# Optimization experiments

Measured on AMD Instinct MI355X. Metric: run time of the kernel, lower is better.

The kernel has to match this reference:

```python
import jax, jax.numpy as jnp
import numpy as np

N, M, H, K, CIN, COUT, P = 50000, 50000, 32, 15, 64, 128, 3
KP_EXTENT = 0.072
RADIUS = 0.06


def setup_inputs() -> dict:
    key = jax.random.key(0)
    ks = jax.random.split(key, 7)
    q_pts = jax.random.uniform(ks[0], (N, P), dtype=jnp.float32) * 0.05
    s_pts = jax.random.uniform(ks[1], (M, P), dtype=jnp.float32) * 0.05
    neighb_inds = jax.random.randint(ks[2], (N, H), 0, M, dtype=jnp.int64)
    x = jax.random.normal(ks[3], (M, CIN), dtype=jnp.float32)
    # kernel points inside sphere of radius RADIUS (stand-in for load_kernels)
    kernel_points = jax.random.normal(ks[4], (K, P), dtype=jnp.float32) * (0.5 * RADIUS)
    stddev = np.sqrt(1.0 / (K * COUT)).astype(np.float32)
    weights = jax.random.normal(ks[5], (K, CIN, COUT), dtype=jnp.float32) * stddev
    bias = jnp.zeros((COUT,), dtype=jnp.float32)
    return {"q_pts": q_pts, "s_pts": s_pts, "neighb_inds": neighb_inds,
            "x": x, "kernel_points": kernel_points, "weights": weights, "bias": bias}


def reference(q_pts, s_pts, neighb_inds, x, kernel_points, weights, bias):
    # pad support points with a far-away point and features with a zero row
    s_pad = jnp.concatenate([s_pts, jnp.full((1, s_pts.shape[1]), 1e6, s_pts.dtype)], axis=0)
    x_pad = jnp.concatenate([x, jnp.zeros((1, x.shape[1]), x.dtype)], axis=0)
    # gather neighbor coords/features: [N, H, P], [N, H, CIN]
    neighbors = s_pad[neighb_inds] - q_pts[:, None, :]
    neighb_x = x_pad[neighb_inds]
    # distances to kernel points: [N, H, K]
    diff = neighbors[:, :, None, :] - kernel_points  # [N, H, K, P]
    sq_d = jnp.sum(diff * diff, axis=-1)
    all_weights = jax.nn.relu(1.0 - jnp.sqrt(sq_d) / KP_EXTENT)  # linear influence
    # aggregate: [N, K, CIN] then apply per-kernel-point weights and sum over K
    weighted_features = jnp.einsum('nhk,nhc->nkc', all_weights, neighb_x)
    out = jnp.einsum('nkc,kco->no', weighted_features, weights) + bias  # [N, COUT]
    return out
```

## Files before the change

kernel.cpp:

```cpp
#include <hip/hip_runtime.h>


#define NPTS   50000
#define NPAD   50048
#define HNB    32
#define KPTS   15
#define CING   64
#define COUTG  128
#define KDIM   960
#define MSUP   50000
#define INV_EXT 13.888889f

#define X2BF_BLKS 1563
#define WT_BLKS   15
#define TWP       72

typedef __attribute__((ext_vector_type(8))) short bf16x8;
typedef __attribute__((ext_vector_type(8))) unsigned short u16x8;
typedef __attribute__((ext_vector_type(4))) float f32x4;

static __device__ __forceinline__ unsigned short f2bf(float f) {
    unsigned int u = __float_as_uint(f);
    u += 0x7FFFu + ((u >> 16) & 1u);
    return (unsigned short)(u >> 16);
}

__global__ __launch_bounds__(256) void kpconv_prep(const float* __restrict__ x,
                                                   unsigned short* __restrict__ xb,
                                                   const float* __restrict__ wgt,
                                                   unsigned short* __restrict__ Wt) {
    __shared__ unsigned short tw[128 * TWP];
    const int tid = threadIdx.x;
    if (blockIdx.x < X2BF_BLKS) {
        int i = (blockIdx.x * 256 + tid) * 8;
        if (i >= MSUP * CING) return;
        float4 a = *(const float4*)(x + i);
        float4 b = *(const float4*)(x + i + 4);
        u16x8 o;
        o[0] = f2bf(a.x); o[1] = f2bf(a.y); o[2] = f2bf(a.z); o[3] = f2bf(a.w);
        o[4] = f2bf(b.x); o[5] = f2bf(b.y); o[6] = f2bf(b.z); o[7] = f2bf(b.w);
        *(u16x8*)(xb + i) = o;
        return;
    }
    const int kc0 = (blockIdx.x - X2BF_BLKS) * 64;
#pragma unroll
    for (int it = 0; it < 32; ++it) {
        int idx = it * 256 + tid;
        int kcl = idx >> 7, o = idx & 127;
        tw[o * TWP + kcl] = f2bf(wgt[(size_t)(kc0 + kcl) * COUTG + o]);
    }
    __syncthreads();
#pragma unroll
    for (int it = 0; it < 4; ++it) {
        int idx = it * 256 + tid;
        int o = idx >> 3, c16 = idx & 7;
        uint4 v = *(const uint4*)&tw[o * TWP + c16 * 8];
        *(uint4*)&Wt[(size_t)o * KDIM + kc0 + c16 * 8] = v;
    }
}

__global__ __launch_bounds__(256, 5) void kpconv_agg4(
    const float* __restrict__ q_pts, const float* __restrict__ s_pts,
    const int* __restrict__ inds, const unsigned short* __restrict__ xb,
    const float* __restrict__ kpts, unsigned short* __restrict__ wf)
{
    __shared__ float4 nb[4 * HNB];

    const int tid  = threadIdx.x;
    const int wav  = tid >> 6;
    const int lane = tid & 63;
    const int l15  = lane & 15;
    const int quad = lane >> 4;
    const int n    = blockIdx.x * 4 + wav;

    if (lane < HNB) {
        int m = inds[n * HNB + lane];
        float qx = q_pts[n * 3 + 0];
        float qy = q_pts[n * 3 + 1];
        float qz = q_pts[n * 3 + 2];
        nb[wav * HNB + lane] = make_float4(s_pts[m * 3 + 0] - qx,
                                           s_pts[m * 3 + 1] - qy,
                                           s_pts[m * 3 + 2] - qz,
                                           __int_as_float(m));
    }
    __syncthreads();

    const bool kvalid = (l15 < KPTS);
    const int  kidx   = kvalid ? l15 : 0;
    const float kx = kpts[kidx * 3 + 0];
    const float ky = kpts[kidx * 3 + 1];
    const float kz = kpts[kidx * 3 + 2];

    bf16x8 af;
    const unsigned short* bj[8];
#pragma unroll
    for (int j = 0; j < 8; ++j) {
        float4 v = nb[wav * HNB + quad * 8 + j];
        bj[j] = xb + (((size_t)__float_as_int(v.w)) << 6) + l15;
        float dx = v.x - kx, dy = v.y - ky, dz = v.z - kz;
        float d  = sqrtf(dx * dx + dy * dy + dz * dz);
        float w  = kvalid ? fmaxf(0.f, 1.f - d * INV_EXT) : 0.f;
        af[j] = (short)f2bf(w);
    }

    unsigned int gv[32];
#pragma unroll
    for (int j = 0; j < 8; ++j)
#pragma unroll
        for (int nt = 0; nt < 4; ++nt)
            gv[j * 4 + nt] = bj[j][nt * 16];
    __builtin_amdgcn_sched_barrier(0);

    f32x4 acc[4];
#pragma unroll
    for (int nt = 0; nt < 4; ++nt) acc[nt] = (f32x4){0.f, 0.f, 0.f, 0.f};

#pragma unroll
    for (int nt = 0; nt < 4; ++nt) {
        union { unsigned int u[4]; bf16x8 f; } pk;
#pragma unroll
        for (int jj = 0; jj < 4; ++jj)
            pk.u[jj] = gv[(2 * jj) * 4 + nt] | (gv[(2 * jj + 1) * 4 + nt] << 16);
        acc[nt] = __builtin_amdgcn_mfma_f32_16x16x32_bf16(pk.f, af, acc[nt], 0, 0, 0);
    }

    if (kvalid) {
        unsigned short* wp = wf + (size_t)n * KDIM + l15 * CING + quad * 4;
#pragma unroll
        for (int nt = 0; nt < 4; ++nt) {
            unsigned int lo = (unsigned)f2bf(acc[nt][0]) | ((unsigned)f2bf(acc[nt][1]) << 16);
            unsigned int hi = (unsigned)f2bf(acc[nt][2]) | ((unsigned)f2bf(acc[nt][3]) << 16);
            *(uint2*)(wp + nt * 16) = make_uint2(lo, hi);
        }
    }
}

#define GBM 64
#define GBK 64
#define GLP 72

__global__ __launch_bounds__(256) void kpconv_gemm2(
    const unsigned short* __restrict__ A,
    const unsigned short* __restrict__ Bt,
    const float* __restrict__ bias,
    float* __restrict__ out)
{
    __shared__ unsigned short As[GBM * GLP];
    __shared__ unsigned short Bs[COUTG * GLP];

    const int tid  = threadIdx.x;
    const int wave = tid >> 6;
    const int lane = tid & 63;
    const int l15  = lane & 15;
    const int quad = lane >> 4;
    const long blockM = (long)blockIdx.x * GBM;

    f32x4 acc[8];
#pragma unroll
    for (int i = 0; i < 8; ++i) acc[i] = (f32x4){0.f, 0.f, 0.f, 0.f};

    const int arow = tid >> 2, acol = (tid & 3) * 16;
    const int brow = tid >> 1, bcol = (tid & 1) * 32;
    const unsigned short* aptr = A + (size_t)(blockM + arow) * KDIM + acol;
    const unsigned short* bptr = Bt + (size_t)brow * KDIM + bcol;

    uint4 ra0 = *(const uint4*)(aptr);
    uint4 ra1 = *(const uint4*)(aptr + 8);
    uint4 rb0 = *(const uint4*)(bptr);
    uint4 rb1 = *(const uint4*)(bptr + 8);
    uint4 rb2 = *(const uint4*)(bptr + 16);
    uint4 rb3 = *(const uint4*)(bptr + 24);

    for (int kk = 0; kk < KDIM; kk += GBK) {
        __syncthreads();
        *(uint4*)&As[arow * GLP + acol]      = ra0;
        *(uint4*)&As[arow * GLP + acol + 8]  = ra1;
        *(uint4*)&Bs[brow * GLP + bcol]      = rb0;
        *(uint4*)&Bs[brow * GLP + bcol + 8]  = rb1;
        *(uint4*)&Bs[brow * GLP + bcol + 16] = rb2;
        *(uint4*)&Bs[brow * GLP + bcol + 24] = rb3;
        __syncthreads();

        if (kk + GBK < KDIM) {
            ra0 = *(const uint4*)(aptr + kk + GBK);
            ra1 = *(const uint4*)(aptr + kk + GBK + 8);
            rb0 = *(const uint4*)(bptr + kk + GBK);
            rb1 = *(const uint4*)(bptr + kk + GBK + 8);
            rb2 = *(const uint4*)(bptr + kk + GBK + 16);
            rb3 = *(const uint4*)(bptr + kk + GBK + 24);
        }

#pragma unroll
        for (int ch = 0; ch < 2; ++ch) {
            bf16x8 afr = *(bf16x8*)&As[(wave * 16 + l15) * GLP + ch * 32 + quad * 8];
#pragma unroll
            for (int nf = 0; nf < 8; ++nf) {
                bf16x8 bfr = *(bf16x8*)&Bs[(nf * 16 + l15) * GLP + ch * 32 + quad * 8];
                acc[nf] = __builtin_amdgcn_mfma_f32_16x16x32_bf16(afr, bfr, acc[nf], 0, 0, 0);
            }
        }
    }

    const long r0 = blockM + wave * 16 + quad * 4;
#pragma unroll
    for (int nf = 0; nf < 8; ++nf) {
        const int col = nf * 16 + l15;
        const float bv = bias[col];
#pragma unroll
        for (int r = 0; r < 4; ++r) {
            long row = r0 + r;
            if (row < NPTS) out[row * COUTG + col] = acc[nf][r] + bv;
        }
    }
}

extern "C" void kernel_launch(void* const* d_in, const int* in_sizes, int n_in,
                              void* d_out, int out_size, void* d_ws, size_t ws_size,
                              hipStream_t stream) {
    const float* q_pts = (const float*)d_in[0];
    const float* s_pts = (const float*)d_in[1];
    const int*   inds  = (const int*)d_in[2];
    const float* x     = (const float*)d_in[3];
    const float* kpts  = (const float*)d_in[4];
    const float* wgt   = (const float*)d_in[5];
    const float* bias  = (const float*)d_in[6];
    float* out = (float*)d_out;

    unsigned short* wfp = (unsigned short*)d_ws;
    unsigned short* xb  = wfp + (size_t)NPAD * KDIM;
    unsigned short* Wt  = xb + (size_t)MSUP * CING;

    kpconv_prep<<<X2BF_BLKS + WT_BLKS, 256, 0, stream>>>(x, xb, wgt, Wt);
    kpconv_agg4<<<NPTS / 4, 256, 0, stream>>>(q_pts, s_pts, inds, xb, kpts, wfp);
    kpconv_gemm2<<<NPAD / GBM, 256, 0, stream>>>(wfp, Wt, bias, out);
}
```

Before: 168.3 us.

## Stage gathered neighbor features into LDS via direct global-to-LDS loads

```diff
diff --git a/kernel.cpp b/kernel.cpp
--- a/kernel.cpp
+++ b/kernel.cpp
@@ -23,6 +23,13 @@
     unsigned int u = __float_as_uint(f);
     u += 0x7FFFu + ((u >> 16) & 1u);
     return (unsigned short)(u >> 16);
+}
+
+static __device__ __forceinline__ void gload_lds16(const unsigned short* g,
+                                                   unsigned short* l) {
+    __builtin_amdgcn_global_load_lds(
+        (const __attribute__((address_space(1))) void*)g,
+        (__attribute__((address_space(3))) void*)l, 16, 0, 0);
 }
 
 __global__ __launch_bounds__(256) void kpconv_prep(const float* __restrict__ x,
@@ -59,12 +66,14 @@
     }
 }
 
-__global__ __launch_bounds__(256, 5) void kpconv_agg4(
+__global__ __launch_bounds__(256, 8) void kpconv_agg5(
     const float* __restrict__ q_pts, const float* __restrict__ s_pts,
     const int* __restrict__ inds, const unsigned short* __restrict__ xb,
     const float* __restrict__ kpts, unsigned short* __restrict__ wf)
 {
     __shared__ float4 nb[4 * HNB];
+    __shared__ int    midx[4 * HNB];
+    __shared__ unsigned short xs[4 * HNB * 64];
 
     const int tid  = threadIdx.x;
     const int wav  = tid >> 6;
@@ -75,15 +84,27 @@
 
     if (lane < HNB) {
         int m = inds[n * HNB + lane];
+        midx[wav * HNB + lane] = m;
         float qx = q_pts[n * 3 + 0];
         float qy = q_pts[n * 3 + 1];
         float qz = q_pts[n * 3 + 2];
         nb[wav * HNB + lane] = make_float4(s_pts[m * 3 + 0] - qx,
                                            s_pts[m * 3 + 1] - qy,
                                            s_pts[m * 3 + 2] - qz,
-                                           __int_as_float(m));
+                                           0.f);
     }
     __syncthreads();
+
+    unsigned short* xsw = &xs[wav * (HNB * 64)];
+    {
+        const int hsub = lane >> 3;
+        const int c0   = (lane & 7) * 8;
+#pragma unroll
+        for (int i = 0; i < 4; ++i) {
+            int m = midx[wav * HNB + i * 8 + hsub];
+            gload_lds16(xb + (((size_t)m) << 6) + c0, xsw + i * 8 * 64);
+        }
+    }
 
     const bool kvalid = (l15 < KPTS);
     const int  kidx   = kvalid ? l15 : 0;
@@ -92,23 +113,16 @@
     const float kz = kpts[kidx * 3 + 2];
 
     bf16x8 af;
-    const unsigned short* bj[8];
 #pragma unroll
     for (int j = 0; j < 8; ++j) {
         float4 v = nb[wav * HNB + quad * 8 + j];
-        bj[j] = xb + (((size_t)__float_as_int(v.w)) << 6) + l15;
         float dx = v.x - kx, dy = v.y - ky, dz = v.z - kz;
         float d  = sqrtf(dx * dx + dy * dy + dz * dz);
         float w  = kvalid ? fmaxf(0.f, 1.f - d * INV_EXT) : 0.f;
         af[j] = (short)f2bf(w);
     }
 
-    unsigned int gv[32];
-#pragma unroll
-    for (int j = 0; j < 8; ++j)
-#pragma unroll
-        for (int nt = 0; nt < 4; ++nt)
-            gv[j * 4 + nt] = bj[j][nt * 16];
+    asm volatile("s_waitcnt vmcnt(0)" ::: "memory");
     __builtin_amdgcn_sched_barrier(0);
 
     f32x4 acc[4];
@@ -119,8 +133,11 @@
     for (int nt = 0; nt < 4; ++nt) {
         union { unsigned int u[4]; bf16x8 f; } pk;
 #pragma unroll
-        for (int jj = 0; jj < 4; ++jj)
-            pk.u[jj] = gv[(2 * jj) * 4 + nt] | (gv[(2 * jj + 1) * 4 + nt] << 16);
+        for (int jj = 0; jj < 4; ++jj) {
+            unsigned int lo = xsw[(quad * 8 + 2 * jj)     * 64 + nt * 16 + l15];
+            unsigned int hi = xsw[(quad * 8 + 2 * jj + 1) * 64 + nt * 16 + l15];
+            pk.u[jj] = lo | (hi << 16);
+        }
         acc[nt] = __builtin_amdgcn_mfma_f32_16x16x32_bf16(pk.f, af, acc[nt], 0, 0, 0);
     }
 
@@ -231,6 +248,6 @@
     unsigned short* Wt  = xb + (size_t)MSUP * CING;
 
     kpconv_prep<<<X2BF_BLKS + WT_BLKS, 256, 0, stream>>>(x, xb, wgt, Wt);
-    kpconv_agg4<<<NPTS / 4, 256, 0, stream>>>(q_pts, s_pts, inds, xb, kpts, wfp);
+    kpconv_agg5<<<NPTS / 4, 256, 0, stream>>>(q_pts, s_pts, inds, xb, kpts, wfp);
     kpconv_gemm2<<<NPAD / GBM, 256, 0, stream>>>(wfp, Wt, bias, out);
 }
```

Result: faster. 162.9 us (-3.2%).
